# Optimization experiments

Measured on AMD Instinct MI355X. Metric: run time of the kernel, lower is better.

Reference implementation:

```python
import jax, jax.numpy as jnp
import numpy as np

NX, NY, NC, NT = 320, 320, 20, 25


def ifft2c(x):
    # centered orthonormal 2D inverse FFT over axes (0,1)
    return jnp.fft.fftshift(
        jnp.fft.ifft2(jnp.fft.ifftshift(x, axes=(0, 1)), axes=(0, 1), norm='ortho'),
        axes=(0, 1))


def warp_bilinear(im, flw):
    # im: [Nx,Ny] complex, flw: [Nx,Ny,2] float pixel displacements
    # Sparse motion matrix application = bilinear gather at (x+u, y+v)
    Nx, Ny = im.shape
    gx, gy = jnp.meshgrid(jnp.arange(Nx, dtype=jnp.float32),
                          jnp.arange(Ny, dtype=jnp.float32), indexing='ij')
    xs = jnp.clip(gx + flw[..., 0], 0.0, Nx - 1.0)
    ys = jnp.clip(gy + flw[..., 1], 0.0, Ny - 1.0)
    x0 = jnp.floor(xs).astype(jnp.int32)
    y0 = jnp.floor(ys).astype(jnp.int32)
    x1 = jnp.minimum(x0 + 1, Nx - 1)
    y1 = jnp.minimum(y0 + 1, Ny - 1)
    wx = xs - x0.astype(jnp.float32)
    wy = ys - y0.astype(jnp.float32)
    return (im[x0, y0] * ((1 - wx) * (1 - wy))
            + im[x1, y0] * (wx * (1 - wy))
            + im[x0, y1] * ((1 - wx) * wy)
            + im[x1, y1] * (wx * wy))


def setup_inputs() -> dict:
    key = jax.random.key(0)
    ks = jax.random.split(key, 6)
    return {
        'kspace_re': jax.random.normal(ks[0], (NX, NY, NC), dtype=jnp.float32),
        'kspace_im': jax.random.normal(ks[1], (NX, NY, NC), dtype=jnp.float32),
        'mask': jax.random.uniform(ks[2], (NX, NY, NC, NT), dtype=jnp.float32),
        'smaps_re': jax.random.normal(ks[3], (NX, NY, NC), dtype=jnp.float32),
        'smaps_im': jax.random.normal(ks[4], (NX, NY, NC), dtype=jnp.float32),
        'flow': jax.random.normal(ks[5], (NX, NY, 2, NT), dtype=jnp.float32),
    }


def reference(kspace_re, kspace_im, mask, smaps_re, smaps_im, flow):
    kspace = kspace_re + 1j * kspace_im          # [Nx,Ny,Nc]
    smaps = smaps_re + 1j * smaps_im             # [Nx,Ny,Nc]
    # masked kspace for all motion states: [Nx,Ny,Nc,Nt]
    ksp_t = kspace[..., None] * mask.astype(kspace.dtype)
    coil_ims = ifft2c(ksp_t)                     # [Nx,Ny,Nc,Nt]
    # coil combine: sum_c ifft2c(k*m) * conj(smaps) -> [Nx,Ny,Nt]
    im_t = jnp.sum(coil_ims * jnp.conj(smaps)[..., None], axis=2)
    # per-frame sparse motion warp, then sum over motion states
    warped = jax.vmap(warp_bilinear, in_axes=(2, 3))(im_t, flow)  # [Nt,Nx,Ny]
    out = jnp.sum(warped, axis=0)                # [Nx,Ny] complex
    return jnp.stack([out.real, out.imag])       # [2,Nx,Ny] float32 view
```

## Files before the change

### kernel.cpp

```cpp
#include <hip/hip_runtime.h>
#include <hip/hip_fp16.h>
#include <math.h>

#define NXY 320
#define NC 20
#define NT 25
#define NPIX 102400
#define PI_F 3.14159265358979f
#define TWOPI_F 6.28318530717959f

__device__ __forceinline__ float2 cmul(float2 a, float2 b) {
    return make_float2(a.x * b.x - a.y * b.y, a.x * b.y + a.y * b.x);
}

struct Tw {
    float2 st[6];
    float  sgn[6];
    float2 w5[5];
    int J;
};

__device__ __forceinline__ void tw_init(Tw& t) {
    const int lane = threadIdx.x & 63;
    #pragma unroll
    for (int s = 0; s < 6; ++s) {
        const int h = 32 >> s;
        const bool up = (lane & h) != 0;
        t.sgn[s] = up ? -1.0f : 1.0f;
        if (up) {
            float ss, cc;
            __sincosf(PI_F * (float)(lane & (h - 1)) / (float)h, &ss, &cc);
            t.st[s] = make_float2(cc, ss);
        } else {
            t.st[s] = make_float2(1.0f, 0.0f);
        }
    }
    t.J = (int)(__brev((unsigned)lane) >> 26);
    t.w5[0] = make_float2(1.0f, 0.0f);
    #pragma unroll
    for (int r = 1; r < 5; ++r) {
        float ss, cc;
        __sincosf(TWOPI_F * (float)(r * t.J) / 320.0f, &ss, &cc);
        t.w5[r] = make_float2(cc, ss);
    }
}

template <int K>
__device__ __forceinline__ void fft320xK(const Tw& t, float2 (&x)[K][5], float2 (&out)[K][5]) {
    #pragma unroll
    for (int s = 0; s < 6; ++s) {
        const int h = 32 >> s;
        #pragma unroll
        for (int r = 0; r < 5; ++r) {
            #pragma unroll
            for (int k = 0; k < K; ++k) {
                float ox = __shfl_xor(x[k][r].x, h);
                float oy = __shfl_xor(x[k][r].y, h);
                float dx = fmaf(t.sgn[s], x[k][r].x, ox);
                float dy = fmaf(t.sgn[s], x[k][r].y, oy);
                x[k][r].x = dx * t.st[s].x - dy * t.st[s].y;
                x[k][r].y = dx * t.st[s].y + dy * t.st[s].x;
            }
        }
    }
    const float W5x[5] = {1.0f, 0.309016994f, -0.809016994f, -0.809016994f, 0.309016994f};
    const float W5y[5] = {0.0f, 0.951056516f, 0.587785252f, -0.587785252f, -0.951056516f};
    #pragma unroll
    for (int k = 0; k < K; ++k) {
        float2 T[5];
        T[0] = x[k][0];
        #pragma unroll
        for (int r = 1; r < 5; ++r) T[r] = cmul(x[k][r], t.w5[r]);
        #pragma unroll
        for (int s5 = 0; s5 < 5; ++s5) {
            float2 acc = T[0];
            #pragma unroll
            for (int r = 1; r < 5; ++r) {
                const int kk = (r * s5) % 5;
                acc.x += T[r].x * W5x[kk] - T[r].y * W5y[kk];
                acc.y += T[r].x * W5y[kk] + T[r].y * W5x[kk];
            }
            out[k][s5] = acc;
        }
    }
}

__global__ __launch_bounds__(256) void k_prep_smaps(const float* __restrict__ smr,
                                                    const float* __restrict__ smi,
                                                    float2* __restrict__ smapsC) {
    const int p0 = blockIdx.x * 64;
    __shared__ float s_r[64 * 21];
    __shared__ float s_i[64 * 21];
    for (int j = threadIdx.x; j < 64 * NC; j += blockDim.x) {
        int p = j / NC, c = j - p * NC;
        s_r[p * 21 + c] = smr[(size_t)p0 * NC + j];
        s_i[p * 21 + c] = smi[(size_t)p0 * NC + j];
    }
    __syncthreads();
    for (int j = threadIdx.x; j < 64 * NC; j += blockDim.x) {
        int c = j >> 6, p = j & 63;
        int pg = p0 + p;
        int m = pg / NXY, n = pg - m * NXY;
        float sgn = (((m + n) & 1) ? -1.0f : 1.0f) * (1.0f / 320.0f);
        smapsC[(size_t)c * NPIX + pg] = make_float2(s_r[p * 21 + c] * sgn,
                                                    -s_i[p * 21 + c] * sgn);
    }
}

__global__ __launch_bounds__(256) void k_perm_smaps(const float2* __restrict__ smapsC,
                                                    __half2* __restrict__ smapsP) {
    const int c = blockIdx.x;
    const int s5 = blockIdx.y;
    const int v0 = blockIdx.z * 64;
    __shared__ __half2 t2[64 * 65];
    for (int j = threadIdx.x; j < 64 * 64; j += blockDim.x) {
        int ur = j >> 6, vc = j & 63;
        float2 v = smapsC[(size_t)c * NPIX + (size_t)(s5 * 64 + ur) * NXY + v0 + vc];
        t2[ur * 65 + vc] = __floats2half2_rn(v.x, v.y);
    }
    __syncthreads();
    for (int j = threadIdx.x; j < 64 * 64; j += blockDim.x) {
        int vr = j >> 6, lane = j & 63;
        int J = (int)(__brev((unsigned)lane) >> 26);
        smapsP[(size_t)((c * NXY + v0 + vr) * 5 + s5) * 64 + lane] = t2[J * 65 + vr];
    }
}

__global__ __launch_bounds__(256) void k_prep_ks(const float* __restrict__ ksr,
                                                 const float* __restrict__ ksi,
                                                 __half2* __restrict__ ksS) {
    const int p0 = blockIdx.x * 64;
    __shared__ float s_r[64 * 21];
    __shared__ float s_i[64 * 21];
    for (int j = threadIdx.x; j < 64 * NC; j += blockDim.x) {
        int p = j / NC, c = j - p * NC;
        s_r[p * 21 + c] = ksr[(size_t)p0 * NC + j];
        s_i[p * 21 + c] = ksi[(size_t)p0 * NC + j];
    }
    __syncthreads();
    for (int j = threadIdx.x; j < 64 * NC; j += blockDim.x) {
        int c = j >> 6, p = j & 63;
        int pg = p0 + p;
        int m = pg / NXY, n = pg - m * NXY;
        float sgn = ((m + n) & 1) ? -1.0f : 1.0f;
        ksS[(size_t)c * NPIX + pg] =
            __floats2half2_rn(s_r[p * 21 + c] * sgn, s_i[p * 21 + c] * sgn);
    }
}

__global__ __launch_bounds__(256) void k_fft_rows(const float* __restrict__ mask,
                                                  const __half2* __restrict__ ksS,
                                                  __half2* __restrict__ Z,
                                                  int t0, int G) {
    const int q = blockIdx.x;
    const int mtile = blockIdx.y;
    const int c = q / G;
    const int tc = q - c * G;
    const int cq = c * NT + t0 + tc;
    const int wave = threadIdx.x >> 6;
    const int lane = threadIdx.x & 63;
    const int m0 = mtile * 16;
    __shared__ __half2 tile[NXY * 17];
    Tw t;
    tw_init(t);
    const __half2* ks_c = ksS + (size_t)c * NPIX;
    const float* mk_c = mask + (size_t)cq;
    float2 x[4][5], out[4][5];
    #pragma unroll
    for (int k = 0; k < 4; ++k) {
        const int pbase = (m0 + wave + 4 * k) * NXY + lane * 5;
        const __half2* kp = ks_c + pbase;
        const float* mp = mk_c + (size_t)pbase * (NC * NT);
        #pragma unroll
        for (int r = 0; r < 5; ++r) {
            float2 kv = __half22float2(kp[r]);
            float mkv = mp[(size_t)r * (NC * NT)];
            x[k][r] = make_float2(kv.x * mkv, kv.y * mkv);
        }
    }
    fft320xK<4>(t, x, out);
    #pragma unroll
    for (int k = 0; k < 4; ++k) {
        const int mm = wave + 4 * k;
        #pragma unroll
        for (int s5 = 0; s5 < 5; ++s5) {
            int v = t.J + 64 * s5;
            tile[v * 17 + mm] = __floats2half2_rn(out[k][s5].x, out[k][s5].y);
        }
    }
    __syncthreads();
    __half2* dst = Z + (size_t)q * NPIX + m0;
    for (int j = threadIdx.x; j < NXY * 16; j += blockDim.x) {
        int mm = j & 15, v = j >> 4;
        dst[(size_t)v * NXY + mm] = tile[v * 17 + mm];
    }
}

__global__ __launch_bounds__(256) void k_fft_cols_combine(const __half2* __restrict__ Z,
                                                          const __half2* __restrict__ smapsP,
                                                          __half2* __restrict__ imtP,
                                                          int t0, int G) {
    const int vtile = blockIdx.x;
    const int tc = blockIdx.y;
    const int half = blockIdx.z;
    const int wave = threadIdx.x >> 6;
    const int lane = threadIdx.x & 63;
    const int v0 = vtile * 8;
    const int vA = v0 + wave;
    const int vB = v0 + 4 + wave;
    __shared__ __half2 tile[NXY * 9];
    Tw t;
    tw_init(t);
    float2 acc[2][5];
    #pragma unroll
    for (int k = 0; k < 2; ++k)
        #pragma unroll
        for (int s5 = 0; s5 < 5; ++s5) acc[k][s5] = make_float2(0.f, 0.f);
    const int c0 = half * 10;
    for (int c = c0; c < c0 + 10; ++c) {
        const __half2* zc = Z + (size_t)(c * G + tc) * NPIX;
        float2 x[2][5], out[2][5];
        const __half2* colA = zc + (size_t)vA * NXY + lane * 5;
        const __half2* colB = zc + (size_t)vB * NXY + lane * 5;
        #pragma unroll
        for (int r = 0; r < 5; ++r) {
            x[0][r] = __half22float2(colA[r]);
            x[1][r] = __half22float2(colB[r]);
        }
        fft320xK<2>(t, x, out);
        const __half2* spA = smapsP + (size_t)((c * NXY + vA) * 5) * 64 + lane;
        const __half2* spB = smapsP + (size_t)((c * NXY + vB) * 5) * 64 + lane;
        #pragma unroll
        for (int s5 = 0; s5 < 5; ++s5) {
            float2 smA = __half22float2(spA[s5 * 64]);
            float2 smB = __half22float2(spB[s5 * 64]);
            float2 ta = cmul(out[0][s5], smA);
            float2 tb = cmul(out[1][s5], smB);
            acc[0][s5].x += ta.x; acc[0][s5].y += ta.y;
            acc[1][s5].x += tb.x; acc[1][s5].y += tb.y;
        }
    }
    #pragma unroll
    for (int s5 = 0; s5 < 5; ++s5) {
        int u = t.J + 64 * s5;
        tile[u * 9 + wave] = __floats2half2_rn(acc[0][s5].x, acc[0][s5].y);
        tile[u * 9 + 4 + wave] = __floats2half2_rn(acc[1][s5].x, acc[1][s5].y);
    }
    __syncthreads();
    __half2* dst = imtP + (size_t)(half * NT + t0 + tc) * NPIX + v0;
    for (int j = threadIdx.x; j < NXY * 8; j += blockDim.x) {
        int vv = j & 7, u = j >> 3;
        dst[(size_t)u * NXY + vv] = tile[u * 9 + vv];
    }
}

__global__ __launch_bounds__(256) void k_warp_sum(const __half2* __restrict__ imtP,
                                                  const float* __restrict__ flow,
                                                  float* __restrict__ out) {
    const int p0 = blockIdx.x * 256;
    const int tid = threadIdx.x;
    __shared__ float s_fl[2 * NT * 257];
    for (int j = tid; j < 256 * 50; j += 256) {
        int pp = j / 50, rem = j - pp * 50;
        int d = rem / 25, tt = rem - d * 25;
        s_fl[(d * NT + tt) * 257 + pp] = flow[(size_t)p0 * 50 + j];
    }
    __syncthreads();
    const int p = p0 + tid;
    const int x = p / NXY, y = p - x * NXY;
    const float fx = (float)x, fy = (float)y;
    float ar = 0.f, ai = 0.f;
    for (int t = 0; t < NT; ++t) {
        float u = s_fl[t * 257 + tid];
        float v = s_fl[(NT + t) * 257 + tid];
        float xs = fminf(fmaxf(fx + u, 0.0f), 319.0f);
        float ys = fminf(fmaxf(fy + v, 0.0f), 319.0f);
        float x0f = floorf(xs), y0f = floorf(ys);
        int x0 = (int)x0f, y0 = (int)y0f;
        int x1 = min(x0 + 1, NXY - 1), y1 = min(y0 + 1, NXY - 1);
        float wx = xs - x0f, wy = ys - y0f;
        const __half2* b0 = imtP + (size_t)t * NPIX;
        const __half2* b1 = imtP + (size_t)(NT + t) * NPIX;
        int i00 = x0 * NXY + y0, i01 = x0 * NXY + y1;
        int i10 = x1 * NXY + y0, i11 = x1 * NXY + y1;
        float2 c00 = __half22float2(b0[i00]); float2 d00 = __half22float2(b1[i00]);
        float2 c01 = __half22float2(b0[i01]); float2 d01 = __half22float2(b1[i01]);
        float2 c10 = __half22float2(b0[i10]); float2 d10 = __half22float2(b1[i10]);
        float2 c11 = __half22float2(b0[i11]); float2 d11 = __half22float2(b1[i11]);
        c00.x += d00.x; c00.y += d00.y;
        c01.x += d01.x; c01.y += d01.y;
        c10.x += d10.x; c10.y += d10.y;
        c11.x += d11.x; c11.y += d11.y;
        float w00 = (1.f - wx) * (1.f - wy), w01 = (1.f - wx) * wy;
        float w10 = wx * (1.f - wy), w11 = wx * wy;
        ar += c00.x * w00 + c01.x * w01 + c10.x * w10 + c11.x * w11;
        ai += c00.y * w00 + c01.y * w01 + c10.y * w10 + c11.y * w11;
    }
    out[p] = ar;
    out[NPIX + p] = ai;
}

extern "C" void kernel_launch(void* const* d_in, const int* in_sizes, int n_in,
                              void* d_out, int out_size, void* d_ws, size_t ws_size,
                              hipStream_t stream) {
    const float* ksr = (const float*)d_in[0];
    const float* ksi = (const float*)d_in[1];
    const float* mask = (const float*)d_in[2];
    const float* smr = (const float*)d_in[3];
    const float* smi = (const float*)d_in[4];
    const float* flow = (const float*)d_in[5];
    float* out = (float*)d_out;

    char* ws = (char*)d_ws;
    const size_t smapsC_bytes = (size_t)NC * NPIX * sizeof(float2);
    const size_t smapsP_bytes = (size_t)NC * NPIX * sizeof(__half2);
    const size_t ksS_bytes = (size_t)NC * NPIX * sizeof(__half2);
    const size_t imtP_bytes = (size_t)2 * NT * NPIX * sizeof(__half2);
    const size_t fixed = smapsC_bytes + smapsP_bytes + ksS_bytes + imtP_bytes;
    const size_t per_t = (size_t)NC * NPIX * sizeof(__half2);

    int G = 1;
    if (ws_size > fixed + per_t) {
        size_t g = (ws_size - fixed) / per_t;
        G = (int)(g > (size_t)NT ? (size_t)NT : g);
    }
    if (G < 1) G = 1;

    float2* smapsC = (float2*)ws;
    __half2* smapsP = (__half2*)(ws + smapsC_bytes);
    __half2* ksS = (__half2*)(ws + smapsC_bytes + smapsP_bytes);
    __half2* imtP = (__half2*)(ws + smapsC_bytes + smapsP_bytes + ksS_bytes);
    __half2* Z = (__half2*)(ws + fixed);

    k_prep_smaps<<<NPIX / 64, 256, 0, stream>>>(smr, smi, smapsC);
    k_perm_smaps<<<dim3(NC, 5, 5), 256, 0, stream>>>(smapsC, smapsP);
    k_prep_ks<<<NPIX / 64, 256, 0, stream>>>(ksr, ksi, ksS);
    for (int t0 = 0; t0 < NT; t0 += G) {
        int g = (NT - t0) < G ? (NT - t0) : G;
        k_fft_rows<<<dim3(NC * g, 20), 256, 0, stream>>>(mask, ksS, Z, t0, g);
        k_fft_cols_combine<<<dim3(40, g, 2), 256, 0, stream>>>(Z, smapsP, imtP, t0, g);
    }
    k_warp_sum<<<NPIX / 256, 256, 0, stream>>>(imtP, flow, out);
}
```

Before: 889.1 us.

## Pre-transpose mask to fp16 per coil-frame layout for coalesced FFT row loads

Adds a kernel that transposes the mask from its pixel-major layout, where coil and frame are innermost, into contiguous fp16 planes per (coil, frame). The row-FFT kernel then reads the mask with unit stride instead of a 2000-byte stride. The goal is to remove the uncoalesced strided global loads of the large mask. The cost is an extra kernel launch, extra workspace, and fp16 rounding of the mask values.

After: 740.8 us. -16.7%, faster.

```diff
diff --git a/kernel.cpp b/kernel.cpp
--- a/kernel.cpp
+++ b/kernel.cpp
@@ -148,15 +148,40 @@
     }
 }
 
-__global__ __launch_bounds__(256) void k_fft_rows(const float* __restrict__ mask,
+__global__ __launch_bounds__(256) void k_transpose_mask(const float* __restrict__ mask,
+                                                        __half* __restrict__ maskT,
+                                                        int t0, int G) {
+    const int p0 = blockIdx.x * 64;
+    const int c = blockIdx.y;
+    __shared__ float tile[64 * 26];
+    if (G == NT) {
+        for (int j = threadIdx.x; j < 64 * NT; j += 256) {
+            int pl = j / NT, tc = j - pl * NT;
+            tile[pl * 26 + tc] = mask[(size_t)(p0 + pl) * (NC * NT) + c * NT + tc];
+        }
+    } else {
+        for (int j = threadIdx.x; j < 64 * G; j += 256) {
+            int pl = j / G, tc = j - pl * G;
+            tile[pl * 26 + tc] = mask[(size_t)(p0 + pl) * (NC * NT) + c * NT + t0 + tc];
+        }
+    }
+    __syncthreads();
+    for (int j = threadIdx.x; j < 16 * G; j += 256) {
+        int p4 = (j & 15) * 4, tc = j >> 4;
+        union { __half2 h2[2]; uint2 u; } pk;
+        pk.h2[0] = __floats2half2_rn(tile[(p4 + 0) * 26 + tc], tile[(p4 + 1) * 26 + tc]);
+        pk.h2[1] = __floats2half2_rn(tile[(p4 + 2) * 26 + tc], tile[(p4 + 3) * 26 + tc]);
+        *reinterpret_cast<uint2*>(maskT + (size_t)(c * G + tc) * NPIX + p0 + p4) = pk.u;
+    }
+}
+
+__global__ __launch_bounds__(256) void k_fft_rows(const __half* __restrict__ maskT,
                                                   const __half2* __restrict__ ksS,
                                                   __half2* __restrict__ Z,
-                                                  int t0, int G) {
+                                                  int G) {
     const int q = blockIdx.x;
     const int mtile = blockIdx.y;
     const int c = q / G;
-    const int tc = q - c * G;
-    const int cq = c * NT + t0 + tc;
     const int wave = threadIdx.x >> 6;
     const int lane = threadIdx.x & 63;
     const int m0 = mtile * 16;
@@ -164,17 +189,17 @@
     Tw t;
     tw_init(t);
     const __half2* ks_c = ksS + (size_t)c * NPIX;
-    const float* mk_c = mask + (size_t)cq;
+    const __half* mk_q = maskT + (size_t)q * NPIX;
     float2 x[4][5], out[4][5];
     #pragma unroll
     for (int k = 0; k < 4; ++k) {
         const int pbase = (m0 + wave + 4 * k) * NXY + lane * 5;
         const __half2* kp = ks_c + pbase;
-        const float* mp = mk_c + (size_t)pbase * (NC * NT);
+        const __half* mp = mk_q + pbase;
         #pragma unroll
         for (int r = 0; r < 5; ++r) {
             float2 kv = __half22float2(kp[r]);
-            float mkv = mp[(size_t)r * (NC * NT)];
+            float mkv = __half2float(mp[r]);
             x[k][r] = make_float2(kv.x * mkv, kv.y * mkv);
         }
     }
@@ -317,7 +342,7 @@
     const size_t ksS_bytes = (size_t)NC * NPIX * sizeof(__half2);
     const size_t imtP_bytes = (size_t)2 * NT * NPIX * sizeof(__half2);
     const size_t fixed = smapsC_bytes + smapsP_bytes + ksS_bytes + imtP_bytes;
-    const size_t per_t = (size_t)NC * NPIX * sizeof(__half2);
+    const size_t per_t = (size_t)NC * NPIX * (sizeof(__half2) + sizeof(__half));
 
     int G = 1;
     if (ws_size > fixed + per_t) {
@@ -331,13 +356,15 @@
     __half2* ksS = (__half2*)(ws + smapsC_bytes + smapsP_bytes);
     __half2* imtP = (__half2*)(ws + smapsC_bytes + smapsP_bytes + ksS_bytes);
     __half2* Z = (__half2*)(ws + fixed);
+    __half* maskT = (__half*)(ws + fixed + (size_t)NC * G * NPIX * sizeof(__half2));
 
     k_prep_smaps<<<NPIX / 64, 256, 0, stream>>>(smr, smi, smapsC);
     k_perm_smaps<<<dim3(NC, 5, 5), 256, 0, stream>>>(smapsC, smapsP);
     k_prep_ks<<<NPIX / 64, 256, 0, stream>>>(ksr, ksi, ksS);
     for (int t0 = 0; t0 < NT; t0 += G) {
         int g = (NT - t0) < G ? (NT - t0) : G;
-        k_fft_rows<<<dim3(NC * g, 20), 256, 0, stream>>>(mask, ksS, Z, t0, g);
+        k_transpose_mask<<<dim3(NPIX / 64, NC), 256, 0, stream>>>(mask, maskT, t0, g);
+        k_fft_rows<<<dim3(NC * g, 20), 256, 0, stream>>>(maskT, ksS, Z, g);
         k_fft_cols_combine<<<dim3(40, g, 2), 256, 0, stream>>>(Z, smapsP, imtP, t0, g);
     }
     k_warp_sum<<<NPIX / 256, 256, 0, stream>>>(imtP, flow, out);
```
